# Optimization experiments

Measured on AMD Instinct MI355X. Metric: run time of the kernel, lower is better.

Reference implementation:

```python
import jax, jax.numpy as jnp
import numpy as np

V = 4
H, W, Z = 32, 64, 13
C = 256
NH = 8
WS = (4, 4, 1)
SS = (2, 2, 0)
HID = 1024


def _layernorm(x, g, b):
    mu = jnp.mean(x, axis=-1, keepdims=True)
    var = jnp.mean((x - mu) ** 2, axis=-1, keepdims=True)
    return (x - mu) * jax.lax.rsqrt(var + 1e-5) * g + b


def setup_inputs() -> dict:
    key = jax.random.key(0)
    ks = jax.random.split(key, 12)
    B = 2
    s = 0.02
    return {
        "x_z": jax.random.normal(ks[0], (B, H, W, Z, C), jnp.float32),
        "x_q": jax.random.normal(ks[1], (B, H, W, Z, C), jnp.float32),
        "x_t": jax.random.normal(ks[2], (B, H, W, Z, C), jnp.float32),
        "x_u": jax.random.normal(ks[3], (B, H, W, Z, C), jnp.float32),
        "qkv_w": jax.random.normal(ks[4], (V, C, 3 * C), jnp.float32) * s,
        "qkv_b": jnp.zeros((V, 3 * C), jnp.float32),
        "proj_w": jax.random.normal(ks[5], (V, C, C), jnp.float32) * s,
        "proj_b": jnp.zeros((V, C), jnp.float32),
        "n1_g": jnp.ones((V, C), jnp.float32),
        "n1_b": jnp.zeros((V, C), jnp.float32),
        "n2_g": jnp.ones((V, C), jnp.float32),
        "n2_b": jnp.zeros((V, C), jnp.float32),
        "fc1_w": jax.random.normal(ks[6], (V, C, HID), jnp.float32) * s,
        "fc1_b": jnp.zeros((V, HID), jnp.float32),
        "fc2_w": jax.random.normal(ks[7], (V, HID, C), jnp.float32) * s,
        "fc2_b": jnp.zeros((V, C), jnp.float32),
    }


def reference(x_z, x_q, x_t, x_u, qkv_w, qkv_b, proj_w, proj_b,
              n1_g, n1_b, n2_g, n2_b, fc1_w, fc1_b, fc2_w, fc2_b):
    x = jnp.stack([x_z, x_q, x_t, x_u], axis=0)  # [V,B,H,W,Z,C]
    B = x.shape[1]
    L = H * W * Z
    w0, w1, w2 = WS
    N = w0 * w1 * w2
    hd = C // NH
    scale = hd ** -0.5

    shortcut = x.reshape(V, B, L, C)
    xn = _layernorm(shortcut, n1_g[:, None, None, :], n1_b[:, None, None, :])
    xs = xn.reshape(V, B, H, W, Z, C)
    # cyclic shift (same sign used for both rolls in the source)
    xs = jnp.roll(xs, shift=SS, axis=(2, 3, 4))
    # window partition -> [V, B_, N, C]
    xw = xs.reshape(V, B, H // w0, w0, W // w1, w1, Z // w2, w2, C)
    xw = xw.transpose(0, 1, 2, 4, 6, 3, 5, 7, 8).reshape(V, -1, N, C)
    B_ = xw.shape[1]

    qkv = jnp.einsum('vbnc,vcd->vbnd', xw, qkv_w) + qkv_b[:, None, None, :]
    qkv = qkv.reshape(V, B_, N, 3, NH, hd).transpose(3, 1, 0, 4, 2, 5)  # [3,B_,V,NH,N,hd]
    q, k, v = qkv[0], qkv[1], qkv[2]
    # per-(variable, head) attention: heads of different variables are concatenated
    attn = jax.nn.softmax(jnp.einsum('bvhnd,bvhmd->bvhnm', q * scale, k), axis=-1)
    ctx = jnp.einsum('bvhnm,bvhmd->bvhnd', attn, v)  # [B_,V,NH,N,hd]
    # faithful to torch reshape (B_, N, V*NH, hd) -> (B_, V*N, C): rows interleave (n, v)
    big = ctx.transpose(0, 3, 1, 2, 4).reshape(B_, V * N, C)
    y = big.reshape(B_, V, N, C).transpose(1, 0, 2, 3)  # slice [:, i*N:(i+1)*N]
    y = jnp.einsum('vbnc,vcd->vbnd', y, proj_w) + proj_b[:, None, None, :]
    # window reverse
    y = y.reshape(V, B, H // w0, W // w1, Z // w2, w0, w1, w2, C)
    y = y.transpose(0, 1, 2, 5, 3, 6, 4, 7, 8).reshape(V, B, H, W, Z, C)
    y = jnp.roll(y, shift=SS, axis=(2, 3, 4))  # same-sign roll (preserves source behavior)
    y = y.reshape(V, B, L, C)

    x2 = shortcut + y
    xm = _layernorm(x2, n2_g[:, None, None, :], n2_b[:, None, None, :])
    h = jax.nn.gelu(jnp.einsum('vblc,vcd->vbld', xm, fc1_w) + fc1_b[:, None, None, :],
                    approximate=False)
    m = jnp.einsum('vbld,vdc->vblc', h, fc2_w) + fc2_b[:, None, None, :]
    out = (x2 + m).reshape(V, B, H, W, Z, C)
    return out  # stacked per-variable outputs in variable_order
```

## Files before the change

### kernel.cpp

```cpp
#include <hip/hip_runtime.h>
#include <hip/hip_bf16.h>
#include <cstdint>
#include <cstddef>

#define DI __device__ __forceinline__

typedef __bf16 bf16_t;
typedef bf16_t bf16x8 __attribute__((ext_vector_type(8)));
typedef float f32x4 __attribute__((ext_vector_type(4)));

constexpr int Vn = 4, Bn = 2, Hn = 32, Wn = 64, Zn = 13, Cn = 256, HIDn = 1024;
constexpr int Ln = Hn * Wn * Zn;
constexpr int BWn = Bn * (Hn / 4) * (Wn / 4) * Zn;
constexpr int PB = Bn * Ln;
constexpr int ROWS = Vn * PB;

DI void gload_lds16(const void* g, void* l) {
  __builtin_amdgcn_global_load_lds(
      (const __attribute__((address_space(1))) void*)g,
      (__attribute__((address_space(3))) void*)l, 16, 0, 0);
}

DI unsigned short f2bf_bits(float f) {
  __hip_bfloat16 h = __float2bfloat16(f);
  return *reinterpret_cast<unsigned short*>(&h);
}

DI float gelu_f(float x) {
  float u = x * x;
  float w = x * fmaf(0.044715f, u, 1.0f);
  float e = __expf(-1.5957691216057308f * w);
  return x * __builtin_amdgcn_rcpf(1.0f + e);
}

__global__ __launch_bounds__(256) void transpose_tile_kernel(
    const float* __restrict__ src, __hip_bfloat16* __restrict__ dst, int K, int N) {
  __shared__ float S[64][65];
  const int n0 = blockIdx.x * 64, k0 = blockIdx.y * 64, v = blockIdx.z;
  const int tc = threadIdx.x & 63, tr = threadIdx.x >> 6;
#pragma unroll
  for (int i = 0; i < 16; ++i) {
    int kk = tr + i * 4;
    S[kk][tc] = src[((size_t)v * K + k0 + kk) * N + n0 + tc];
  }
  __syncthreads();
#pragma unroll
  for (int i = 0; i < 16; ++i) {
    int nn = tr + i * 4;
    dst[((size_t)v * N + n0 + nn) * K + k0 + tc] = __float2bfloat16(S[tc][nn]);
  }
}

__global__ __launch_bounds__(256) void ln1_kernel(
    const float* __restrict__ x0, const float* __restrict__ x1,
    const float* __restrict__ x2i, const float* __restrict__ x3,
    const float* __restrict__ g_, const float* __restrict__ b_,
    __hip_bfloat16* __restrict__ xw) {
  int gw = blockIdx.x * 4 + (threadIdx.x >> 6);
  int lane = threadIdx.x & 63;
  int v = gw / PB;
  int rem = gw - v * PB;
  int bw = rem >> 4, nn = rem & 15;
  int zb = bw % 13;
  int t = bw / 13;
  int wb = t & 15, t2 = t >> 4;
  int hb = t2 & 7, b = t2 >> 3;
  int hs = (hb * 4 + (nn >> 2) + 30) & 31;
  int wsrc = (wb * 4 + (nn & 3) + 62) & 63;
  size_t l = (size_t)(hs * 64 + wsrc) * 13 + zb;
  const float* xv = (v == 0) ? x0 : (v == 1) ? x1 : (v == 2) ? x2i : x3;
  const float* xp = xv + ((size_t)b * Ln + l) * 256;
  float4 val = *(const float4*)(xp + lane * 4);
  float s = val.x + val.y + val.z + val.w;
  float sq = val.x * val.x + val.y * val.y + val.z * val.z + val.w * val.w;
#pragma unroll
  for (int o = 32; o; o >>= 1) {
    s += __shfl_xor(s, o);
    sq += __shfl_xor(sq, o);
  }
  float mean = s * (1.0f / 256.0f);
  float var = sq * (1.0f / 256.0f) - mean * mean;
  float rstd = rsqrtf(var + 1e-5f);
  const float* gg = g_ + v * 256 + lane * 4;
  const float* bb = b_ + v * 256 + lane * 4;
  ushort4 o4;
  o4.x = f2bf_bits((val.x - mean) * rstd * gg[0] + bb[0]);
  o4.y = f2bf_bits((val.y - mean) * rstd * gg[1] + bb[1]);
  o4.z = f2bf_bits((val.z - mean) * rstd * gg[2] + bb[2]);
  o4.w = f2bf_bits((val.w - mean) * rstd * gg[3] + bb[3]);
  *reinterpret_cast<ushort4*>(xw + (size_t)gw * 256 + lane * 4) = o4;
}

__global__ __launch_bounds__(256) void ln2_kernel(
    const float* __restrict__ x2, const float* __restrict__ g_,
    const float* __restrict__ b_, __hip_bfloat16* __restrict__ xm) {
  int r = blockIdx.x * 4 + (threadIdx.x >> 6);
  int lane = threadIdx.x & 63;
  int v = r / PB;
  const float* xp = x2 + (size_t)r * 256;
  float4 val = *(const float4*)(xp + lane * 4);
  float s = val.x + val.y + val.z + val.w;
  float sq = val.x * val.x + val.y * val.y + val.z * val.z + val.w * val.w;
#pragma unroll
  for (int o = 32; o; o >>= 1) {
    s += __shfl_xor(s, o);
    sq += __shfl_xor(sq, o);
  }
  float mean = s * (1.0f / 256.0f);
  float var = sq * (1.0f / 256.0f) - mean * mean;
  float rstd = rsqrtf(var + 1e-5f);
  const float* gg = g_ + v * 256 + lane * 4;
  const float* bb = b_ + v * 256 + lane * 4;
  ushort4 o4;
  o4.x = f2bf_bits((val.x - mean) * rstd * gg[0] + bb[0]);
  o4.y = f2bf_bits((val.y - mean) * rstd * gg[1] + bb[1]);
  o4.z = f2bf_bits((val.z - mean) * rstd * gg[2] + bb[2]);
  o4.w = f2bf_bits((val.w - mean) * rstd * gg[3] + bb[3]);
  *reinterpret_cast<ushort4*>(xm + (size_t)r * 256 + lane * 4) = o4;
}

__global__ __launch_bounds__(256) void attn_kernel(
    const __hip_bfloat16* __restrict__ qkvp, __hip_bfloat16* __restrict__ ctx) {
  __shared__ float P[4][16][17];
  int b_ = blockIdx.x;
  int v = blockIdx.y;
  int wid = threadIdx.x >> 6, lane = threadIdx.x & 63;
  int lm = lane & 15, hi = lane >> 4;
  const bf16_t* base = (const bf16_t*)qkvp + (size_t)(v * BWn + b_) * 16 * 768;
  const float scale = 0.17677669529663687f;
  f32x4 zero = {0.f, 0.f, 0.f, 0.f};
#pragma unroll
  for (int hh = 0; hh < 2; ++hh) {
    int h = wid + 4 * hh;
    bf16x8 qf = *(const bf16x8*)(base + (size_t)lm * 768 + h * 32 + hi * 8);
    bf16x8 kf = *(const bf16x8*)(base + (size_t)lm * 768 + 256 + h * 32 + hi * 8);
    f32x4 s = __builtin_amdgcn_mfma_f32_16x16x32_bf16(qf, kf, zero, 0, 0, 0);
    float p0[4];
#pragma unroll
    for (int q = 0; q < 4; ++q) {
      float val = s[q] * scale;
      float mx = val;
#pragma unroll
      for (int o = 8; o >= 1; o >>= 1) mx = fmaxf(mx, __shfl_xor(mx, o));
      float e = __expf(val - mx);
      float sum = e;
#pragma unroll
      for (int o = 8; o >= 1; o >>= 1) sum += __shfl_xor(sum, o);
      p0[q] = e * __builtin_amdgcn_rcpf(sum);
    }
#pragma unroll
    for (int q = 0; q < 4; ++q) P[wid][hi * 4 + q][lm] = p0[q];
    bf16x8 pa;
#pragma unroll
    for (int j = 0; j < 8; ++j) pa[j] = (bf16_t)0.f;
    if (hi < 2) {
#pragma unroll
      for (int j = 0; j < 8; ++j) pa[j] = (bf16_t)P[wid][lm][hi * 8 + j];
    }
#pragma unroll
    for (int dh = 0; dh < 2; ++dh) {
      bf16x8 vf;
#pragma unroll
      for (int j = 0; j < 8; ++j) vf[j] = (bf16_t)0.f;
      if (hi < 2) {
#pragma unroll
        for (int j = 0; j < 8; ++j)
          vf[j] = base[(size_t)(hi * 8 + j) * 768 + 512 + h * 32 + dh * 16 + lm];
      }
      f32x4 c = __builtin_amdgcn_mfma_f32_16x16x32_bf16(pa, vf, zero, 0, 0, 0);
#pragma unroll
      for (int q = 0; q < 4; ++q) {
        int n = hi * 4 + q;
        int d = dh * 16 + lm;
        int r = n * 4 + v;
        int vo = r >> 4, no = r & 15;
        ctx[((size_t)(vo * BWn + b_) * 16 + no) * 256 + h * 32 + d] = __float2bfloat16(c[q]);
      }
    }
  }
}

template <int EPI, int K, int N>
__global__ __launch_bounds__(256, 3) void gemm4(
    const __hip_bfloat16* __restrict__ A, const __hip_bfloat16* __restrict__ WT,
    const float* __restrict__ bias, __hip_bfloat16* __restrict__ outb,
    float* __restrict__ outf, const float* __restrict__ xi0,
    const float* __restrict__ xi1, const float* __restrict__ xi2,
    const float* __restrict__ xi3) {
  constexpr int NT = K / 64;
  constexpr int NC = N / 128;
  const int v = blockIdx.z;
  const int x = blockIdx.x;
  const int xcd = x & 7;
  const int j = x >> 3;
  const int c = j % NC;
  const int r = xcd + 8 * (j / NC);
  const int rowBase = r * 128;
  const int colBase = c * 128;

  const bf16_t* Av = (const bf16_t*)A + ((size_t)v * PB + rowBase) * K;
  const bf16_t* Wv = (const bf16_t*)WT + ((size_t)v * N + colBase) * K;

  __shared__ __align__(16) uint8_t smem[40960];
  bf16_t(*As)[64] = (bf16_t(*)[64])smem;
  bf16_t(*Bs)[64] = (bf16_t(*)[64])(smem + 16384);

  const int tid = threadIdx.x, wid = tid >> 6, lane = tid & 63;
  const int wr = wid >> 1, wc = wid & 1;
  const int lm = lane & 15, hi = lane >> 4;
  const int rA = lane >> 3;
  const int lg = (lane & 7) ^ rA;

  f32x4 acc[4][4];
#pragma unroll
  for (int m = 0; m < 4; ++m)
#pragma unroll
    for (int n = 0; n < 4; ++n) acc[m][n] = f32x4{0.f, 0.f, 0.f, 0.f};

  for (int t = 0; t < NT; ++t) {
    if (t) __syncthreads();
#pragma unroll
    for (int g = 0; g < 4; ++g) {
      int grp = wid * 4 + g;
      gload_lds16(Av + (size_t)(grp * 8 + rA) * K + t * 64 + lg * 8, &As[grp * 8][0]);
    }
#pragma unroll
    for (int g = 0; g < 4; ++g) {
      int grp = wid * 4 + g;
      gload_lds16(Wv + (size_t)(grp * 8 + rA) * K + t * 64 + lg * 8, &Bs[grp * 8][0]);
    }
    __syncthreads();
#pragma unroll
    for (int kk = 0; kk < 2; ++kk) {
      bf16x8 af[4], bfv[4];
#pragma unroll
      for (int m = 0; m < 4; ++m) {
        const int rr = wr * 64 + m * 16 + lm;
        af[m] = *(const bf16x8*)&As[rr][((kk * 4 + hi) ^ (lm & 7)) * 8];
      }
#pragma unroll
      for (int n = 0; n < 4; ++n) {
        const int rr = wc * 64 + n * 16 + lm;
        bfv[n] = *(const bf16x8*)&Bs[rr][((kk * 4 + hi) ^ (lm & 7)) * 8];
      }
#pragma unroll
      for (int m = 0; m < 4; ++m)
#pragma unroll
        for (int n = 0; n < 4; ++n)
          acc[m][n] = __builtin_amdgcn_mfma_f32_16x16x32_bf16(af[m], bfv[n], acc[m][n], 0, 0, 0);
    }
  }

  __syncthreads();
  uint8_t* ep = smem + wid * 10240;

  if constexpr (EPI == 0 || EPI == 2) {
    ushort(*E)[72] = (ushort(*)[72])ep;
    float bcol[4];
#pragma unroll
    for (int n = 0; n < 4; ++n) bcol[n] = bias[v * N + colBase + wc * 64 + n * 16 + lm];
#pragma unroll
    for (int m = 0; m < 4; ++m)
#pragma unroll
      for (int q = 0; q < 4; ++q) {
        int lr = m * 16 + hi * 4 + q;
#pragma unroll
        for (int n = 0; n < 4; ++n) {
          float val = acc[m][n][q] + bcol[n];
          if constexpr (EPI == 2) val = gelu_f(val);
          E[lr][n * 16 + lm] = f2bf_bits(val);
        }
      }
    const int pr = lane >> 3, pc = lane & 7;
#pragma unroll
    for (int p = 0; p < 8; ++p) {
      int lr = p * 8 + pr;
      bf16x8 val = *(const bf16x8*)&E[lr][pc * 8];
      size_t grow = (size_t)v * PB + rowBase + wr * 64 + lr;
      int gcol = colBase + wc * 64 + pc * 8;
      *(bf16x8*)&outb[grow * N + gcol] = val;
    }
  } else {
    float(*F)[36] = (float(*)[36])ep;
    const int pr = lane >> 3, pc = lane & 7;
#pragma unroll
    for (int h2 = 0; h2 < 2; ++h2) {
#pragma unroll
      for (int m = 0; m < 4; ++m)
#pragma unroll
        for (int q = 0; q < 4; ++q) {
          int lr = m * 16 + hi * 4 + q;
#pragma unroll
          for (int n2 = 0; n2 < 2; ++n2) F[lr][n2 * 16 + lm] = acc[m][h2 * 2 + n2][q];
        }
#pragma unroll
      for (int p = 0; p < 8; ++p) {
        int lr = p * 8 + pr;
        f32x4 a4 = *(const f32x4*)&F[lr][pc * 4];
        int rowv = rowBase + wr * 64 + lr;
        int gcol = colBase + wc * 64 + h2 * 32 + pc * 4;
        f32x4 b4 = *(const f32x4*)&bias[v * N + gcol];
        if constexpr (EPI == 1) {
          int b_ = rowv >> 4, nn = rowv & 15;
          int zb = b_ % 13;
          int tt = b_ / 13;
          int wb = tt & 15, tt2 = tt >> 4;
          int hb = tt2 & 7, bb = tt2 >> 3;
          int h2v = (hb * 4 + (nn >> 2) + 2) & 31;
          int w2v = (wb * 4 + (nn & 3) + 2) & 63;
          size_t l = (size_t)(h2v * 64 + w2v) * 13 + zb;
          const float* xv = (v == 0) ? xi0 : (v == 1) ? xi1 : (v == 2) ? xi2 : xi3;
          f32x4 x4 = *(const f32x4*)(xv + ((size_t)bb * Ln + l) * 256 + gcol);
          f32x4 o4 = a4 + b4 + x4;
          *(f32x4*)(outf + (((size_t)v * Bn + bb) * Ln + l) * 256 + gcol) = o4;
        } else {
          float* o = outf + ((size_t)v * PB + rowv) * 256 + gcol;
          f32x4 cur = *(const f32x4*)o;
          f32x4 o4 = cur + a4 + b4;
          *(f32x4*)o = o4;
        }
      }
      if (h2 == 0) __builtin_amdgcn_s_waitcnt(0);
    }
  }
}

extern "C" void kernel_launch(void* const* d_in, const int* in_sizes, int n_in,
                              void* d_out, int out_size, void* d_ws, size_t ws_size,
                              hipStream_t stream) {
  const float* x0 = (const float*)d_in[0];
  const float* x1 = (const float*)d_in[1];
  const float* x2i = (const float*)d_in[2];
  const float* x3 = (const float*)d_in[3];
  const float* qkv_w = (const float*)d_in[4];
  const float* qkv_b = (const float*)d_in[5];
  const float* proj_w = (const float*)d_in[6];
  const float* proj_b = (const float*)d_in[7];
  const float* n1g = (const float*)d_in[8];
  const float* n1b = (const float*)d_in[9];
  const float* n2g = (const float*)d_in[10];
  const float* n2b = (const float*)d_in[11];
  const float* fc1_w = (const float*)d_in[12];
  const float* fc1_b = (const float*)d_in[13];
  const float* fc2_w = (const float*)d_in[14];
  const float* fc2_b = (const float*)d_in[15];
  float* out = (float*)d_out;

  uint8_t* ws = (uint8_t*)d_ws;
  size_t off = 0;
  auto alloc = [&](size_t bytes) -> void* {
    void* p = ws + off;
    off += (bytes + 255) & ~(size_t)255;
    return p;
  };
  __hip_bfloat16* wqkvT = (__hip_bfloat16*)alloc((size_t)Vn * Cn * 768 * 2);
  __hip_bfloat16* wprojT = (__hip_bfloat16*)alloc((size_t)Vn * Cn * Cn * 2);
  __hip_bfloat16* wfc1T = (__hip_bfloat16*)alloc((size_t)Vn * Cn * HIDn * 2);
  __hip_bfloat16* wfc2T = (__hip_bfloat16*)alloc((size_t)Vn * HIDn * Cn * 2);
  __hip_bfloat16* xw = (__hip_bfloat16*)alloc((size_t)ROWS * Cn * 2);
  __hip_bfloat16* qkvb = (__hip_bfloat16*)alloc((size_t)ROWS * HIDn * 2);

  transpose_tile_kernel<<<dim3(768 / 64, 256 / 64, Vn), 256, 0, stream>>>(qkv_w, wqkvT, 256, 768);
  transpose_tile_kernel<<<dim3(256 / 64, 256 / 64, Vn), 256, 0, stream>>>(proj_w, wprojT, 256, 256);
  transpose_tile_kernel<<<dim3(1024 / 64, 256 / 64, Vn), 256, 0, stream>>>(fc1_w, wfc1T, 256, 1024);
  transpose_tile_kernel<<<dim3(256 / 64, 1024 / 64, Vn), 256, 0, stream>>>(fc2_w, wfc2T, 1024, 256);

  ln1_kernel<<<ROWS / 4, 256, 0, stream>>>(x0, x1, x2i, x3, n1g, n1b, xw);

  gemm4<0, 256, 768><<<dim3(416 * 6, 1, Vn), 256, 0, stream>>>(
      xw, wqkvT, qkv_b, qkvb, nullptr, nullptr, nullptr, nullptr, nullptr);

  attn_kernel<<<dim3(BWn, Vn), 256, 0, stream>>>(qkvb, xw );

  gemm4<1, 256, 256><<<dim3(416 * 2, 1, Vn), 256, 0, stream>>>(
      xw , wprojT, proj_b, nullptr, out , x0, x1, x2i, x3);

  ln2_kernel<<<ROWS / 4, 256, 0, stream>>>(out , n2g, n2b, xw );

  gemm4<2, 256, 1024><<<dim3(416 * 8, 1, Vn), 256, 0, stream>>>(
      xw , wfc1T, fc1_b, qkvb , nullptr, nullptr, nullptr, nullptr, nullptr);

  gemm4<3, 1024, 256><<<dim3(416 * 2, 1, Vn), 256, 0, stream>>>(
      qkvb , wfc2T, fc2_b, nullptr, out, nullptr, nullptr, nullptr, nullptr);
}
```

Measured before the change: 924.6 us.

## Widen GEMM tiles to 128x256 with 512-thread blocks

The GEMM kernel moves from 128x128 tiles with 4 waves to 128x256 tiles with 8 waves. Each A tile is now reused across twice as many output columns, which cuts global A traffic and halves the block count. The epilogue is split into two phases of 32 rows so it fits the per-wave LDS slice, and the explicit waitcnt between halves is dropped. Bigger blocks and launch bounds of 4 may raise register pressure and lower occupancy flexibility.

```diff
diff --git a/kernel.cpp b/kernel.cpp
--- a/kernel.cpp
+++ b/kernel.cpp
@@ -181,14 +181,14 @@
 }
 
 template <int EPI, int K, int N>
-__global__ __launch_bounds__(256, 3) void gemm4(
+__global__ __launch_bounds__(512, 4) void gemm5(
     const __hip_bfloat16* __restrict__ A, const __hip_bfloat16* __restrict__ WT,
     const float* __restrict__ bias, __hip_bfloat16* __restrict__ outb,
     float* __restrict__ outf, const float* __restrict__ xi0,
     const float* __restrict__ xi1, const float* __restrict__ xi2,
     const float* __restrict__ xi3) {
   constexpr int NT = K / 64;
-  constexpr int NC = N / 128;
+  constexpr int NC = N / 256;
   const int v = blockIdx.z;
   const int x = blockIdx.x;
   const int xcd = x & 7;
@@ -196,17 +196,17 @@
   const int c = j % NC;
   const int r = xcd + 8 * (j / NC);
   const int rowBase = r * 128;
-  const int colBase = c * 128;
+  const int colBase = c * 256;
 
   const bf16_t* Av = (const bf16_t*)A + ((size_t)v * PB + rowBase) * K;
   const bf16_t* Wv = (const bf16_t*)WT + ((size_t)v * N + colBase) * K;
 
-  __shared__ __align__(16) uint8_t smem[40960];
+  __shared__ __align__(16) uint8_t smem[49152];
   bf16_t(*As)[64] = (bf16_t(*)[64])smem;
   bf16_t(*Bs)[64] = (bf16_t(*)[64])(smem + 16384);
 
   const int tid = threadIdx.x, wid = tid >> 6, lane = tid & 63;
-  const int wr = wid >> 1, wc = wid & 1;
+  const int wr = wid >> 2, wc = wid & 3;
   const int lm = lane & 15, hi = lane >> 4;
   const int rA = lane >> 3;
   const int lg = (lane & 7) ^ rA;
@@ -220,8 +220,8 @@
   for (int t = 0; t < NT; ++t) {
     if (t) __syncthreads();
 #pragma unroll
-    for (int g = 0; g < 4; ++g) {
-      int grp = wid * 4 + g;
+    for (int g = 0; g < 2; ++g) {
+      int grp = wid * 2 + g;
       gload_lds16(Av + (size_t)(grp * 8 + rA) * K + t * 64 + lg * 8, &As[grp * 8][0]);
     }
 #pragma unroll
@@ -252,7 +252,8 @@
   }
 
   __syncthreads();
-  uint8_t* ep = smem + wid * 10240;
+  uint8_t* ep = smem + wid * 6144;
+  const int pr = lane >> 3, pc = lane & 7;
 
   if constexpr (EPI == 0 || EPI == 2) {
     ushort(*E)[72] = (ushort(*)[72])ep;
@@ -260,67 +261,74 @@
 #pragma unroll
     for (int n = 0; n < 4; ++n) bcol[n] = bias[v * N + colBase + wc * 64 + n * 16 + lm];
 #pragma unroll
-    for (int m = 0; m < 4; ++m)
-#pragma unroll
-      for (int q = 0; q < 4; ++q) {
-        int lr = m * 16 + hi * 4 + q;
-#pragma unroll
-        for (int n = 0; n < 4; ++n) {
-          float val = acc[m][n][q] + bcol[n];
-          if constexpr (EPI == 2) val = gelu_f(val);
-          E[lr][n * 16 + lm] = f2bf_bits(val);
+    for (int ph = 0; ph < 2; ++ph) {
+#pragma unroll
+      for (int mm = 0; mm < 2; ++mm) {
+        int m = ph * 2 + mm;
+#pragma unroll
+        for (int q = 0; q < 4; ++q) {
+          int lr = mm * 16 + hi * 4 + q;
+#pragma unroll
+          for (int n = 0; n < 4; ++n) {
+            float val = acc[m][n][q] + bcol[n];
+            if constexpr (EPI == 2) val = gelu_f(val);
+            E[lr][n * 16 + lm] = f2bf_bits(val);
+          }
         }
       }
-    const int pr = lane >> 3, pc = lane & 7;
-#pragma unroll
-    for (int p = 0; p < 8; ++p) {
-      int lr = p * 8 + pr;
-      bf16x8 val = *(const bf16x8*)&E[lr][pc * 8];
-      size_t grow = (size_t)v * PB + rowBase + wr * 64 + lr;
-      int gcol = colBase + wc * 64 + pc * 8;
-      *(bf16x8*)&outb[grow * N + gcol] = val;
+#pragma unroll
+      for (int p = 0; p < 4; ++p) {
+        int lr = p * 8 + pr;
+        bf16x8 valv = *(const bf16x8*)&E[lr][pc * 8];
+        size_t grow = (size_t)v * PB + rowBase + wr * 64 + ph * 32 + lr;
+        int gcol = colBase + wc * 64 + pc * 8;
+        *(bf16x8*)&outb[grow * N + gcol] = valv;
+      }
     }
   } else {
     float(*F)[36] = (float(*)[36])ep;
-    const int pr = lane >> 3, pc = lane & 7;
-#pragma unroll
-    for (int h2 = 0; h2 < 2; ++h2) {
-#pragma unroll
-      for (int m = 0; m < 4; ++m)
-#pragma unroll
-        for (int q = 0; q < 4; ++q) {
-          int lr = m * 16 + hi * 4 + q;
-#pragma unroll
-          for (int n2 = 0; n2 < 2; ++n2) F[lr][n2 * 16 + lm] = acc[m][h2 * 2 + n2][q];
+#pragma unroll
+    for (int ph = 0; ph < 2; ++ph) {
+#pragma unroll
+      for (int h2 = 0; h2 < 2; ++h2) {
+#pragma unroll
+        for (int mm = 0; mm < 2; ++mm) {
+          int m = ph * 2 + mm;
+#pragma unroll
+          for (int q = 0; q < 4; ++q) {
+            int lr = mm * 16 + hi * 4 + q;
+#pragma unroll
+            for (int n2 = 0; n2 < 2; ++n2) F[lr][n2 * 16 + lm] = acc[m][h2 * 2 + n2][q];
+          }
         }
 #pragma unroll
-      for (int p = 0; p < 8; ++p) {
-        int lr = p * 8 + pr;
-        f32x4 a4 = *(const f32x4*)&F[lr][pc * 4];
-        int rowv = rowBase + wr * 64 + lr;
-        int gcol = colBase + wc * 64 + h2 * 32 + pc * 4;
-        f32x4 b4 = *(const f32x4*)&bias[v * N + gcol];
-        if constexpr (EPI == 1) {
-          int b_ = rowv >> 4, nn = rowv & 15;
-          int zb = b_ % 13;
-          int tt = b_ / 13;
-          int wb = tt & 15, tt2 = tt >> 4;
-          int hb = tt2 & 7, bb = tt2 >> 3;
-          int h2v = (hb * 4 + (nn >> 2) + 2) & 31;
-          int w2v = (wb * 4 + (nn & 3) + 2) & 63;
-          size_t l = (size_t)(h2v * 64 + w2v) * 13 + zb;
-          const float* xv = (v == 0) ? xi0 : (v == 1) ? xi1 : (v == 2) ? xi2 : xi3;
-          f32x4 x4 = *(const f32x4*)(xv + ((size_t)bb * Ln + l) * 256 + gcol);
-          f32x4 o4 = a4 + b4 + x4;
-          *(f32x4*)(outf + (((size_t)v * Bn + bb) * Ln + l) * 256 + gcol) = o4;
-        } else {
-          float* o = outf + ((size_t)v * PB + rowv) * 256 + gcol;
-          f32x4 cur = *(const f32x4*)o;
-          f32x4 o4 = cur + a4 + b4;
-          *(f32x4*)o = o4;
+        for (int p = 0; p < 4; ++p) {
+          int lr = p * 8 + pr;
+          f32x4 a4 = *(const f32x4*)&F[lr][pc * 4];
+          int rowv = rowBase + wr * 64 + ph * 32 + lr;
+          int gcol = colBase + wc * 64 + h2 * 32 + pc * 4;
+          f32x4 b4 = *(const f32x4*)&bias[v * N + gcol];
+          if constexpr (EPI == 1) {
+            int b_ = rowv >> 4, nn = rowv & 15;
+            int zb = b_ % 13;
+            int tt = b_ / 13;
+            int wb = tt & 15, tt2 = tt >> 4;
+            int hb = tt2 & 7, bb = tt2 >> 3;
+            int h2v = (hb * 4 + (nn >> 2) + 2) & 31;
+            int w2v = (wb * 4 + (nn & 3) + 2) & 63;
+            size_t l = (size_t)(h2v * 64 + w2v) * 13 + zb;
+            const float* xv = (v == 0) ? xi0 : (v == 1) ? xi1 : (v == 2) ? xi2 : xi3;
+            f32x4 x4 = *(const f32x4*)(xv + ((size_t)bb * Ln + l) * 256 + gcol);
+            f32x4 o4 = a4 + b4 + x4;
+            *(f32x4*)(outf + (((size_t)v * Bn + bb) * Ln + l) * 256 + gcol) = o4;
+          } else {
+            float* o = outf + ((size_t)v * PB + rowv) * 256 + gcol;
+            f32x4 cur = *(const f32x4*)o;
+            f32x4 o4 = cur + a4 + b4;
+            *(f32x4*)o = o4;
+          }
         }
       }
-      if (h2 == 0) __builtin_amdgcn_s_waitcnt(0);
     }
   }
 }
@@ -367,19 +375,19 @@
 
   ln1_kernel<<<ROWS / 4, 256, 0, stream>>>(x0, x1, x2i, x3, n1g, n1b, xw);
 
-  gemm4<0, 256, 768><<<dim3(416 * 6, 1, Vn), 256, 0, stream>>>(
+  gemm5<0, 256, 768><<<dim3(416 * 3, 1, Vn), 512, 0, stream>>>(
       xw, wqkvT, qkv_b, qkvb, nullptr, nullptr, nullptr, nullptr, nullptr);
 
   attn_kernel<<<dim3(BWn, Vn), 256, 0, stream>>>(qkvb, xw );
 
-  gemm4<1, 256, 256><<<dim3(416 * 2, 1, Vn), 256, 0, stream>>>(
+  gemm5<1, 256, 256><<<dim3(416, 1, Vn), 512, 0, stream>>>(
       xw , wprojT, proj_b, nullptr, out , x0, x1, x2i, x3);
 
   ln2_kernel<<<ROWS / 4, 256, 0, stream>>>(out , n2g, n2b, xw );
 
-  gemm4<2, 256, 1024><<<dim3(416 * 8, 1, Vn), 256, 0, stream>>>(
+  gemm5<2, 256, 1024><<<dim3(416 * 4, 1, Vn), 512, 0, stream>>>(
       xw , wfc1T, fc1_b, qkvb , nullptr, nullptr, nullptr, nullptr, nullptr);
 
-  gemm4<3, 1024, 256><<<dim3(416 * 2, 1, Vn), 256, 0, stream>>>(
+  gemm5<3, 1024, 256><<<dim3(416, 1, Vn), 512, 0, stream>>>(
       qkvb , wfc2T, fc2_b, nullptr, out, nullptr, nullptr, nullptr, nullptr);
 }
```

After: 1.007 ms. +8.9%, slower.

## Fuse LayerNorm2, FC1+GELU and FC2 into one MLP kernel

Applied to the files above, without the earlier changes.

Replaces the separate ln2 kernel and two MLP GEMMs with one kernel. Each 512-thread block normalizes 128 rows into LDS, computes the hidden layer in 128-column chunks with GELU kept in LDS, and accumulates FC2 into registers. This removes the global round trip of the 1024-wide bf16 hidden activation and two launches. In exchange it uses 128KB of LDS, which limits each CU to one block, and runs with little overlap between weight loads and MFMA because every stage is separated by barriers.

```diff
diff --git a/kernel.cpp b/kernel.cpp
--- a/kernel.cpp
+++ b/kernel.cpp
@@ -91,34 +91,6 @@
   *reinterpret_cast<ushort4*>(xw + (size_t)gw * 256 + lane * 4) = o4;
 }
 
-__global__ __launch_bounds__(256) void ln2_kernel(
-    const float* __restrict__ x2, const float* __restrict__ g_,
-    const float* __restrict__ b_, __hip_bfloat16* __restrict__ xm) {
-  int r = blockIdx.x * 4 + (threadIdx.x >> 6);
-  int lane = threadIdx.x & 63;
-  int v = r / PB;
-  const float* xp = x2 + (size_t)r * 256;
-  float4 val = *(const float4*)(xp + lane * 4);
-  float s = val.x + val.y + val.z + val.w;
-  float sq = val.x * val.x + val.y * val.y + val.z * val.z + val.w * val.w;
-#pragma unroll
-  for (int o = 32; o; o >>= 1) {
-    s += __shfl_xor(s, o);
-    sq += __shfl_xor(sq, o);
-  }
-  float mean = s * (1.0f / 256.0f);
-  float var = sq * (1.0f / 256.0f) - mean * mean;
-  float rstd = rsqrtf(var + 1e-5f);
-  const float* gg = g_ + v * 256 + lane * 4;
-  const float* bb = b_ + v * 256 + lane * 4;
-  ushort4 o4;
-  o4.x = f2bf_bits((val.x - mean) * rstd * gg[0] + bb[0]);
-  o4.y = f2bf_bits((val.y - mean) * rstd * gg[1] + bb[1]);
-  o4.z = f2bf_bits((val.z - mean) * rstd * gg[2] + bb[2]);
-  o4.w = f2bf_bits((val.w - mean) * rstd * gg[3] + bb[3]);
-  *reinterpret_cast<ushort4*>(xm + (size_t)r * 256 + lane * 4) = o4;
-}
-
 __global__ __launch_bounds__(256) void attn_kernel(
     const __hip_bfloat16* __restrict__ qkvp, __hip_bfloat16* __restrict__ ctx) {
   __shared__ float P[4][16][17];
@@ -254,7 +226,7 @@
   __syncthreads();
   uint8_t* ep = smem + wid * 10240;
 
-  if constexpr (EPI == 0 || EPI == 2) {
+  if constexpr (EPI == 0) {
     ushort(*E)[72] = (ushort(*)[72])ep;
     float bcol[4];
 #pragma unroll
@@ -265,11 +237,7 @@
       for (int q = 0; q < 4; ++q) {
         int lr = m * 16 + hi * 4 + q;
 #pragma unroll
-        for (int n = 0; n < 4; ++n) {
-          float val = acc[m][n][q] + bcol[n];
-          if constexpr (EPI == 2) val = gelu_f(val);
-          E[lr][n * 16 + lm] = f2bf_bits(val);
-        }
+        for (int n = 0; n < 4; ++n) E[lr][n * 16 + lm] = f2bf_bits(acc[m][n][q] + bcol[n]);
       }
     const int pr = lane >> 3, pc = lane & 7;
 #pragma unroll
@@ -300,28 +268,219 @@
         int rowv = rowBase + wr * 64 + lr;
         int gcol = colBase + wc * 64 + h2 * 32 + pc * 4;
         f32x4 b4 = *(const f32x4*)&bias[v * N + gcol];
-        if constexpr (EPI == 1) {
-          int b_ = rowv >> 4, nn = rowv & 15;
-          int zb = b_ % 13;
-          int tt = b_ / 13;
-          int wb = tt & 15, tt2 = tt >> 4;
-          int hb = tt2 & 7, bb = tt2 >> 3;
-          int h2v = (hb * 4 + (nn >> 2) + 2) & 31;
-          int w2v = (wb * 4 + (nn & 3) + 2) & 63;
-          size_t l = (size_t)(h2v * 64 + w2v) * 13 + zb;
-          const float* xv = (v == 0) ? xi0 : (v == 1) ? xi1 : (v == 2) ? xi2 : xi3;
-          f32x4 x4 = *(const f32x4*)(xv + ((size_t)bb * Ln + l) * 256 + gcol);
-          f32x4 o4 = a4 + b4 + x4;
-          *(f32x4*)(outf + (((size_t)v * Bn + bb) * Ln + l) * 256 + gcol) = o4;
-        } else {
-          float* o = outf + ((size_t)v * PB + rowv) * 256 + gcol;
-          f32x4 cur = *(const f32x4*)o;
-          f32x4 o4 = cur + a4 + b4;
-          *(f32x4*)o = o4;
+        int b_ = rowv >> 4, nn = rowv & 15;
+        int zb = b_ % 13;
+        int tt = b_ / 13;
+        int wb = tt & 15, tt2 = tt >> 4;
+        int hb = tt2 & 7, bb = tt2 >> 3;
+        int h2v = (hb * 4 + (nn >> 2) + 2) & 31;
+        int w2v = (wb * 4 + (nn & 3) + 2) & 63;
+        size_t l = (size_t)(h2v * 64 + w2v) * 13 + zb;
+        const float* xv = (v == 0) ? xi0 : (v == 1) ? xi1 : (v == 2) ? xi2 : xi3;
+        f32x4 x4 = *(const f32x4*)(xv + ((size_t)bb * Ln + l) * 256 + gcol);
+        f32x4 o4 = a4 + b4 + x4;
+        *(f32x4*)(outf + (((size_t)v * Bn + bb) * Ln + l) * 256 + gcol) = o4;
+      }
+      if (h2 == 0) __builtin_amdgcn_s_waitcnt(0);
+    }
+  }
+}
+
+__global__ __launch_bounds__(512, 1) void mlp_fused(
+    const float* __restrict__ x2,
+    const __hip_bfloat16* __restrict__ W1T,
+    const __hip_bfloat16* __restrict__ W2T,
+    const float* __restrict__ b1, const float* __restrict__ b2,
+    const float* __restrict__ g2, const float* __restrict__ bt2,
+    float* __restrict__ outp) {
+  const int v = blockIdx.z;
+  const size_t gRow0 = (size_t)v * PB + (size_t)blockIdx.x * 128;
+
+  __shared__ __align__(16) uint8_t smem[131072];
+  uint8_t* regA = smem;
+  uint8_t* regH = smem + 65536;
+  uint8_t* regC = smem + 98304;
+
+  const int tid = threadIdx.x, wid = tid >> 6, lane = tid & 63;
+  const int lm = lane & 15, hi = lane >> 4;
+  const int wr = wid >> 1;
+  const int wc = wid & 1;
+
+  const float* gg = g2 + v * 256;
+  const float* gb = bt2 + v * 256;
+  {
+    float g4[4], b4l[4];
+#pragma unroll
+    for (int e = 0; e < 4; ++e) { g4[e] = gg[lane * 4 + e]; b4l[e] = gb[lane * 4 + e]; }
+    for (int i = 0; i < 16; ++i) {
+      int row = wid * 16 + i;
+      const float* xp = x2 + (gRow0 + row) * 256;
+      float4 val = *(const float4*)(xp + lane * 4);
+      float s = val.x + val.y + val.z + val.w;
+      float sq = val.x * val.x + val.y * val.y + val.z * val.z + val.w * val.w;
+#pragma unroll
+      for (int o = 32; o; o >>= 1) {
+        s += __shfl_xor(s, o);
+        sq += __shfl_xor(sq, o);
+      }
+      float mean = s * (1.0f / 256.0f);
+      float var = sq * (1.0f / 256.0f) - mean * mean;
+      float rstd = rsqrtf(var + 1e-5f);
+      ushort4 o4;
+      o4.x = f2bf_bits((val.x - mean) * rstd * g4[0] + b4l[0]);
+      o4.y = f2bf_bits((val.y - mean) * rstd * g4[1] + b4l[1]);
+      o4.z = f2bf_bits((val.z - mean) * rstd * g4[2] + b4l[2]);
+      o4.w = f2bf_bits((val.w - mean) * rstd * g4[3] + b4l[3]);
+      int pg = (lane >> 1) ^ (row & 7);
+      *(ushort4*)(regA + row * 512 + pg * 16 + (lane & 1) * 8) = o4;
+    }
+  }
+  __syncthreads();
+
+  bf16x8 afx[2][4][2];
+#pragma unroll
+  for (int mm = 0; mm < 2; ++mm)
+#pragma unroll
+    for (int t = 0; t < 4; ++t)
+#pragma unroll
+      for (int kk = 0; kk < 2; ++kk) {
+        int row = wr * 32 + mm * 16 + lm;
+        int g = t * 8 + kk * 4 + hi;
+        int pg = g ^ (row & 7);
+        afx[mm][t][kk] = *(const bf16x8*)(regA + row * 512 + pg * 16);
+      }
+  __syncthreads();
+
+  f32x4 acc2[2][8];
+#pragma unroll
+  for (int mm = 0; mm < 2; ++mm)
+#pragma unroll
+    for (int nn = 0; nn < 8; ++nn) acc2[mm][nn] = f32x4{0.f, 0.f, 0.f, 0.f};
+
+  const bf16_t* W1v = (const bf16_t*)W1T + (size_t)v * 1024 * 256;
+  const bf16_t* W2v = (const bf16_t*)W2T + (size_t)v * 256 * 1024;
+
+  for (int hc = 0; hc < 8; ++hc) {
+#pragma unroll
+    for (int rd = 0; rd < 8; ++rd) {
+      int s = (rd * 8 + wid) * 64 + lane;
+      int row = s >> 5, pg = s & 31;
+      int g = pg ^ (row & 7);
+      gload_lds16(W1v + (size_t)(hc * 128 + row) * 256 + g * 8, regA + (rd * 8 + wid) * 1024);
+    }
+#pragma unroll
+    for (int rd = 0; rd < 4; ++rd) {
+      int s = (rd * 8 + wid) * 64 + lane;
+      int col = s >> 3, pg = s & 7;
+      int g = pg ^ (col & 7);
+      gload_lds16(W2v + (size_t)col * 1024 + hc * 128 + g * 8, regC + (rd * 8 + wid) * 1024);
+    }
+    __syncthreads();
+
+    f32x4 acc1[2][4];
+#pragma unroll
+    for (int mm = 0; mm < 2; ++mm)
+#pragma unroll
+      for (int nn = 0; nn < 4; ++nn) acc1[mm][nn] = f32x4{0.f, 0.f, 0.f, 0.f};
+#pragma unroll
+    for (int t = 0; t < 4; ++t)
+#pragma unroll
+      for (int kk = 0; kk < 2; ++kk) {
+        bf16x8 wf[4];
+#pragma unroll
+        for (int nn = 0; nn < 4; ++nn) {
+          int row = wc * 64 + nn * 16 + lm;
+          int g = t * 8 + kk * 4 + hi;
+          int pg = g ^ (row & 7);
+          wf[nn] = *(const bf16x8*)(regA + row * 512 + pg * 16);
         }
-      }
-      if (h2 == 0) __builtin_amdgcn_s_waitcnt(0);
-    }
+#pragma unroll
+        for (int mm = 0; mm < 2; ++mm)
+#pragma unroll
+          for (int nn = 0; nn < 4; ++nn)
+            acc1[mm][nn] =
+                __builtin_amdgcn_mfma_f32_16x16x32_bf16(afx[mm][t][kk], wf[nn], acc1[mm][nn], 0, 0, 0);
+      }
+
+    float b1c[4];
+#pragma unroll
+    for (int nn = 0; nn < 4; ++nn) b1c[nn] = b1[v * 1024 + hc * 128 + wc * 64 + nn * 16 + lm];
+#pragma unroll
+    for (int mm = 0; mm < 2; ++mm)
+#pragma unroll
+      for (int nn = 0; nn < 4; ++nn)
+#pragma unroll
+        for (int q = 0; q < 4; ++q) {
+          int row = wr * 32 + mm * 16 + hi * 4 + q;
+          int col = wc * 64 + nn * 16 + lm;
+          float val = gelu_f(acc1[mm][nn][q] + b1c[nn]);
+          int pg = (col >> 3) ^ (row & 7);
+          *(ushort*)(regH + row * 256 + pg * 16 + (col & 7) * 2) = f2bf_bits(val);
+        }
+    __syncthreads();
+
+#pragma unroll
+    for (int t2 = 0; t2 < 2; ++t2) {
+      if (t2 == 1) {
+        __syncthreads();
+#pragma unroll
+        for (int rd = 0; rd < 4; ++rd) {
+          int s = (rd * 8 + wid) * 64 + lane;
+          int col = s >> 3, pg = s & 7;
+          int g = pg ^ (col & 7);
+          gload_lds16(W2v + (size_t)col * 1024 + hc * 128 + 64 + g * 8, regC + (rd * 8 + wid) * 1024);
+        }
+        __syncthreads();
+      }
+#pragma unroll
+      for (int kk = 0; kk < 2; ++kk) {
+        bf16x8 hf[2];
+#pragma unroll
+        for (int mm = 0; mm < 2; ++mm) {
+          int row = wr * 32 + mm * 16 + lm;
+          int g = t2 * 8 + kk * 4 + hi;
+          int pg = g ^ (row & 7);
+          hf[mm] = *(const bf16x8*)(regH + row * 256 + pg * 16);
+        }
+#pragma unroll
+        for (int nn = 0; nn < 8; ++nn) {
+          int col = wc * 128 + nn * 16 + lm;
+          int g = kk * 4 + hi;
+          int pg = g ^ (col & 7);
+          bf16x8 w2f = *(const bf16x8*)(regC + col * 128 + pg * 16);
+#pragma unroll
+          for (int mm = 0; mm < 2; ++mm)
+            acc2[mm][nn] = __builtin_amdgcn_mfma_f32_16x16x32_bf16(hf[mm], w2f, acc2[mm][nn], 0, 0, 0);
+        }
+      }
+    }
+    __syncthreads();
+  }
+
+  float(*F)[36] = (float(*)[36])(smem + wid * 8192);
+  const int pr = lane >> 3, pc = lane & 7;
+#pragma unroll
+  for (int ps = 0; ps < 4; ++ps) {
+#pragma unroll
+    for (int mm = 0; mm < 2; ++mm)
+#pragma unroll
+      for (int q = 0; q < 4; ++q) {
+        int lr = mm * 16 + hi * 4 + q;
+#pragma unroll
+        for (int n2 = 0; n2 < 2; ++n2) F[lr][n2 * 16 + lm] = acc2[mm][ps * 2 + n2][q];
+      }
+#pragma unroll
+    for (int p = 0; p < 4; ++p) {
+      int lr = p * 8 + pr;
+      f32x4 a4 = *(const f32x4*)&F[lr][pc * 4];
+      size_t grow = gRow0 + wr * 32 + lr;
+      int gcol = wc * 128 + ps * 32 + pc * 4;
+      f32x4 b4 = *(const f32x4*)&b2[v * 256 + gcol];
+      float* o = outp + grow * 256 + gcol;
+      f32x4 cur = *(const f32x4*)o;
+      *(f32x4*)o = cur + a4 + b4;
+    }
+    __builtin_amdgcn_s_waitcnt(0);
   }
 }
 
@@ -358,7 +517,7 @@
   __hip_bfloat16* wfc1T = (__hip_bfloat16*)alloc((size_t)Vn * Cn * HIDn * 2);
   __hip_bfloat16* wfc2T = (__hip_bfloat16*)alloc((size_t)Vn * HIDn * Cn * 2);
   __hip_bfloat16* xw = (__hip_bfloat16*)alloc((size_t)ROWS * Cn * 2);
-  __hip_bfloat16* qkvb = (__hip_bfloat16*)alloc((size_t)ROWS * HIDn * 2);
+  __hip_bfloat16* qkvb = (__hip_bfloat16*)alloc((size_t)ROWS * 768 * 2);
 
   transpose_tile_kernel<<<dim3(768 / 64, 256 / 64, Vn), 256, 0, stream>>>(qkv_w, wqkvT, 256, 768);
   transpose_tile_kernel<<<dim3(256 / 64, 256 / 64, Vn), 256, 0, stream>>>(proj_w, wprojT, 256, 256);
@@ -375,11 +534,6 @@
   gemm4<1, 256, 256><<<dim3(416 * 2, 1, Vn), 256, 0, stream>>>(
       xw , wprojT, proj_b, nullptr, out , x0, x1, x2i, x3);
 
-  ln2_kernel<<<ROWS / 4, 256, 0, stream>>>(out , n2g, n2b, xw );
-
-  gemm4<2, 256, 1024><<<dim3(416 * 8, 1, Vn), 256, 0, stream>>>(
-      xw , wfc1T, fc1_b, qkvb , nullptr, nullptr, nullptr, nullptr, nullptr);
-
-  gemm4<3, 1024, 256><<<dim3(416 * 2, 1, Vn), 256, 0, stream>>>(
-      qkvb , wfc2T, fc2_b, nullptr, out, nullptr, nullptr, nullptr, nullptr);
-}
+  mlp_fused<<<dim3(416, 1, Vn), 512, 0, stream>>>(
+      out , wfc1T, wfc2T, fc1_b, fc2_b, n2g, n2b, out);
+}
```

Result: no change. 919.0 us (-0.6%).

## Fuse LN2, FC1+GELU and FC2 into a single MLP kernel

Applied to the files above, without the earlier changes.

Replaces the separate ln2 kernel and the two MLP GEMM launches with one kernel. Each block normalizes 64 rows into LDS, then loops over 32-wide hidden chunks, computing FC1+GELU into LDS and accumulating FC2 in registers. The bf16 hidden activation no longer makes a round trip through global memory, and two launches go away. In exchange, every block re-streams the full FC1 and FC2 weights in small chunks with several barriers per chunk. The FC1 tiles are only 16x16 per wave, so MFMA utilization and latency hiding may be worse than in the tiled GEMMs.

```diff
diff --git a/kernel.cpp b/kernel.cpp
--- a/kernel.cpp
+++ b/kernel.cpp
@@ -91,34 +91,6 @@
   *reinterpret_cast<ushort4*>(xw + (size_t)gw * 256 + lane * 4) = o4;
 }
 
-__global__ __launch_bounds__(256) void ln2_kernel(
-    const float* __restrict__ x2, const float* __restrict__ g_,
-    const float* __restrict__ b_, __hip_bfloat16* __restrict__ xm) {
-  int r = blockIdx.x * 4 + (threadIdx.x >> 6);
-  int lane = threadIdx.x & 63;
-  int v = r / PB;
-  const float* xp = x2 + (size_t)r * 256;
-  float4 val = *(const float4*)(xp + lane * 4);
-  float s = val.x + val.y + val.z + val.w;
-  float sq = val.x * val.x + val.y * val.y + val.z * val.z + val.w * val.w;
-#pragma unroll
-  for (int o = 32; o; o >>= 1) {
-    s += __shfl_xor(s, o);
-    sq += __shfl_xor(sq, o);
-  }
-  float mean = s * (1.0f / 256.0f);
-  float var = sq * (1.0f / 256.0f) - mean * mean;
-  float rstd = rsqrtf(var + 1e-5f);
-  const float* gg = g_ + v * 256 + lane * 4;
-  const float* bb = b_ + v * 256 + lane * 4;
-  ushort4 o4;
-  o4.x = f2bf_bits((val.x - mean) * rstd * gg[0] + bb[0]);
-  o4.y = f2bf_bits((val.y - mean) * rstd * gg[1] + bb[1]);
-  o4.z = f2bf_bits((val.z - mean) * rstd * gg[2] + bb[2]);
-  o4.w = f2bf_bits((val.w - mean) * rstd * gg[3] + bb[3]);
-  *reinterpret_cast<ushort4*>(xm + (size_t)r * 256 + lane * 4) = o4;
-}
-
 __global__ __launch_bounds__(256) void attn_kernel(
     const __hip_bfloat16* __restrict__ qkvp, __hip_bfloat16* __restrict__ ctx) {
   __shared__ float P[4][16][17];
@@ -254,7 +226,7 @@
   __syncthreads();
   uint8_t* ep = smem + wid * 10240;
 
-  if constexpr (EPI == 0 || EPI == 2) {
+  if constexpr (EPI == 0) {
     ushort(*E)[72] = (ushort(*)[72])ep;
     float bcol[4];
 #pragma unroll
@@ -265,11 +237,7 @@
       for (int q = 0; q < 4; ++q) {
         int lr = m * 16 + hi * 4 + q;
 #pragma unroll
-        for (int n = 0; n < 4; ++n) {
-          float val = acc[m][n][q] + bcol[n];
-          if constexpr (EPI == 2) val = gelu_f(val);
-          E[lr][n * 16 + lm] = f2bf_bits(val);
-        }
+        for (int n = 0; n < 4; ++n) E[lr][n * 16 + lm] = f2bf_bits(acc[m][n][q] + bcol[n]);
       }
     const int pr = lane >> 3, pc = lane & 7;
 #pragma unroll
@@ -300,27 +268,170 @@
         int rowv = rowBase + wr * 64 + lr;
         int gcol = colBase + wc * 64 + h2 * 32 + pc * 4;
         f32x4 b4 = *(const f32x4*)&bias[v * N + gcol];
-        if constexpr (EPI == 1) {
-          int b_ = rowv >> 4, nn = rowv & 15;
-          int zb = b_ % 13;
-          int tt = b_ / 13;
-          int wb = tt & 15, tt2 = tt >> 4;
-          int hb = tt2 & 7, bb = tt2 >> 3;
-          int h2v = (hb * 4 + (nn >> 2) + 2) & 31;
-          int w2v = (wb * 4 + (nn & 3) + 2) & 63;
-          size_t l = (size_t)(h2v * 64 + w2v) * 13 + zb;
-          const float* xv = (v == 0) ? xi0 : (v == 1) ? xi1 : (v == 2) ? xi2 : xi3;
-          f32x4 x4 = *(const f32x4*)(xv + ((size_t)bb * Ln + l) * 256 + gcol);
-          f32x4 o4 = a4 + b4 + x4;
-          *(f32x4*)(outf + (((size_t)v * Bn + bb) * Ln + l) * 256 + gcol) = o4;
-        } else {
-          float* o = outf + ((size_t)v * PB + rowv) * 256 + gcol;
-          f32x4 cur = *(const f32x4*)o;
-          f32x4 o4 = cur + a4 + b4;
-          *(f32x4*)o = o4;
-        }
+        int b_ = rowv >> 4, nn = rowv & 15;
+        int zb = b_ % 13;
+        int tt = b_ / 13;
+        int wb = tt & 15, tt2 = tt >> 4;
+        int hb = tt2 & 7, bb = tt2 >> 3;
+        int h2v = (hb * 4 + (nn >> 2) + 2) & 31;
+        int w2v = (wb * 4 + (nn & 3) + 2) & 63;
+        size_t l = (size_t)(h2v * 64 + w2v) * 13 + zb;
+        const float* xv = (v == 0) ? xi0 : (v == 1) ? xi1 : (v == 2) ? xi2 : xi3;
+        f32x4 x4 = *(const f32x4*)(xv + ((size_t)bb * Ln + l) * 256 + gcol);
+        f32x4 o4 = a4 + b4 + x4;
+        *(f32x4*)(outf + (((size_t)v * Bn + bb) * Ln + l) * 256 + gcol) = o4;
       }
       if (h2 == 0) __builtin_amdgcn_s_waitcnt(0);
+    }
+  }
+}
+
+__global__ __launch_bounds__(512, 4) void mlp_fused2(
+    const float* __restrict__ x2,
+    const __hip_bfloat16* __restrict__ W1T,
+    const __hip_bfloat16* __restrict__ W2T,
+    const float* __restrict__ b1, const float* __restrict__ b2,
+    const float* __restrict__ g2, const float* __restrict__ bt2,
+    float* __restrict__ outp) {
+  const int v = blockIdx.z;
+  const size_t gRow0 = (size_t)v * PB + (size_t)blockIdx.x * 64;
+
+  __shared__ __align__(16) uint8_t smem[69632];
+  uint8_t* W1c = smem + 32768;
+  uint8_t* W2c = smem + 49152;
+  uint8_t* hbuf = smem + 65536;
+
+  const int tid = threadIdx.x, wid = tid >> 6, lane = tid & 63;
+  const int lm = lane & 15, hi = lane >> 4;
+  const int wa = wid >> 2;
+  const int wb = wid & 3;
+
+  {
+    const float* gg = g2 + v * 256;
+    const float* gb = bt2 + v * 256;
+    float g4[4], b4l[4];
+#pragma unroll
+    for (int e = 0; e < 4; ++e) { g4[e] = gg[lane * 4 + e]; b4l[e] = gb[lane * 4 + e]; }
+    for (int i = 0; i < 8; ++i) {
+      int row = wid * 8 + i;
+      const float* xp = x2 + (gRow0 + row) * 256;
+      float4 val = *(const float4*)(xp + lane * 4);
+      float s = val.x + val.y + val.z + val.w;
+      float sq = val.x * val.x + val.y * val.y + val.z * val.z + val.w * val.w;
+#pragma unroll
+      for (int o = 32; o; o >>= 1) {
+        s += __shfl_xor(s, o);
+        sq += __shfl_xor(sq, o);
+      }
+      float mean = s * (1.0f / 256.0f);
+      float var = sq * (1.0f / 256.0f) - mean * mean;
+      float rstd = rsqrtf(var + 1e-5f);
+      ushort4 o4;
+      o4.x = f2bf_bits((val.x - mean) * rstd * g4[0] + b4l[0]);
+      o4.y = f2bf_bits((val.y - mean) * rstd * g4[1] + b4l[1]);
+      o4.z = f2bf_bits((val.z - mean) * rstd * g4[2] + b4l[2]);
+      o4.w = f2bf_bits((val.w - mean) * rstd * g4[3] + b4l[3]);
+      int t = hi;
+      int g = (lane >> 1) & 7;
+      int p = row * 4 + t;
+      int gp = g ^ ((row & 1) * 4 + t);
+      *(ushort4*)(smem + p * 128 + gp * 16 + (lane & 1) * 8) = o4;
+    }
+  }
+  __syncthreads();
+
+  bf16x8 xnf[4][2];
+#pragma unroll
+  for (int t = 0; t < 4; ++t)
+#pragma unroll
+    for (int kk = 0; kk < 2; ++kk) {
+      int row = wb * 16 + lm;
+      int p = row * 4 + t;
+      int gp = (kk * 4 + hi) ^ ((row & 1) * 4 + t);
+      xnf[t][kk] = *(const bf16x8*)(smem + p * 128 + gp * 16);
+    }
+
+  f32x4 acc2[8];
+#pragma unroll
+  for (int ca = 0; ca < 8; ++ca) acc2[ca] = f32x4{0.f, 0.f, 0.f, 0.f};
+
+  const bf16_t* W1v = (const bf16_t*)W1T + (size_t)v * 1024 * 256;
+  const bf16_t* W2v = (const bf16_t*)W2T + (size_t)v * 256 * 1024;
+  const int l8 = lane >> 3;
+  const int lg = (lane & 7) ^ l8;
+
+  for (int hc = 0; hc < 32; ++hc) {
+    if (hc) __syncthreads();
+#pragma unroll
+    for (int s = 0; s < 2; ++s) {
+      int i = wid * 2 + s;
+      int p = i * 8 + l8;
+      gload_lds16(W1v + (size_t)(hc * 32 + (p >> 2)) * 256 + (p & 3) * 64 + lg * 8,
+                  W1c + i * 1024);
+    }
+#pragma unroll
+    for (int s = 0; s < 2; ++s) {
+      int i = wid * 2 + s;
+      int p = i * 8 + l8;
+      gload_lds16(W2v + (size_t)(p * 2 + (lg >> 2)) * 1024 + hc * 32 + (lg & 3) * 8,
+                  W2c + i * 1024);
+    }
+    __syncthreads();
+
+    f32x4 acc1 = f32x4{0.f, 0.f, 0.f, 0.f};
+#pragma unroll
+    for (int t = 0; t < 4; ++t)
+#pragma unroll
+      for (int kk = 0; kk < 2; ++kk) {
+        int hrow = wa * 16 + lm;
+        int p = hrow * 4 + t;
+        int gp = (kk * 4 + hi) ^ ((hrow & 1) * 4 + t);
+        bf16x8 w1f = *(const bf16x8*)(W1c + p * 128 + gp * 16);
+        acc1 = __builtin_amdgcn_mfma_f32_16x16x32_bf16(w1f, xnf[t][kk], acc1, 0, 0, 0);
+      }
+
+    {
+      f32x4 b1v = *(const f32x4*)&b1[v * 1024 + hc * 32 + wa * 16 + hi * 4];
+      ushort4 hp;
+      hp.x = f2bf_bits(gelu_f(acc1[0] + b1v[0]));
+      hp.y = f2bf_bits(gelu_f(acc1[1] + b1v[1]));
+      hp.z = f2bf_bits(gelu_f(acc1[2] + b1v[2]));
+      hp.w = f2bf_bits(gelu_f(acc1[3] + b1v[3]));
+      int row = wb * 16 + lm;
+      int p = row >> 1;
+      int gl = (row & 1) * 4 + wa * 2 + (hi >> 1);
+      int gp = gl ^ (p & 7);
+      *(ushort4*)(hbuf + p * 128 + gp * 16 + (hi & 1) * 8) = hp;
+    }
+    __syncthreads();
+
+    {
+      int row = wb * 16 + lm;
+      int p = row >> 1;
+      int gp = ((row & 1) * 4 + hi) ^ (p & 7);
+      bf16x8 hf = *(const bf16x8*)(hbuf + p * 128 + gp * 16);
+#pragma unroll
+      for (int ca = 0; ca < 8; ++ca) {
+        int col = wa * 128 + ca * 16 + lm;
+        int p2 = col >> 1;
+        int gp2 = ((col & 1) * 4 + hi) ^ (p2 & 7);
+        bf16x8 w2f = *(const bf16x8*)(W2c + p2 * 128 + gp2 * 16);
+        acc2[ca] = __builtin_amdgcn_mfma_f32_16x16x32_bf16(w2f, hf, acc2[ca], 0, 0, 0);
+      }
+    }
+  }
+
+  {
+    size_t orow = gRow0 + wb * 16 + lm;
+    float* obase = outp + orow * 256;
+#pragma unroll
+    for (int ca = 0; ca < 8; ++ca) {
+      int col = wa * 128 + ca * 16 + hi * 4;
+      f32x4 b4 = *(const f32x4*)&b2[v * 256 + col];
+      float* o = obase + col;
+      f32x4 cur = *(const f32x4*)o;
+      f32x4 res = cur + acc2[ca] + b4;
+      *(f32x4*)o = res;
     }
   }
 }
@@ -358,7 +469,7 @@
   __hip_bfloat16* wfc1T = (__hip_bfloat16*)alloc((size_t)Vn * Cn * HIDn * 2);
   __hip_bfloat16* wfc2T = (__hip_bfloat16*)alloc((size_t)Vn * HIDn * Cn * 2);
   __hip_bfloat16* xw = (__hip_bfloat16*)alloc((size_t)ROWS * Cn * 2);
-  __hip_bfloat16* qkvb = (__hip_bfloat16*)alloc((size_t)ROWS * HIDn * 2);
+  __hip_bfloat16* qkvb = (__hip_bfloat16*)alloc((size_t)ROWS * 768 * 2);
 
   transpose_tile_kernel<<<dim3(768 / 64, 256 / 64, Vn), 256, 0, stream>>>(qkv_w, wqkvT, 256, 768);
   transpose_tile_kernel<<<dim3(256 / 64, 256 / 64, Vn), 256, 0, stream>>>(proj_w, wprojT, 256, 256);
@@ -375,11 +486,6 @@
   gemm4<1, 256, 256><<<dim3(416 * 2, 1, Vn), 256, 0, stream>>>(
       xw , wprojT, proj_b, nullptr, out , x0, x1, x2i, x3);
 
-  ln2_kernel<<<ROWS / 4, 256, 0, stream>>>(out , n2g, n2b, xw );
-
-  gemm4<2, 256, 1024><<<dim3(416 * 8, 1, Vn), 256, 0, stream>>>(
-      xw , wfc1T, fc1_b, qkvb , nullptr, nullptr, nullptr, nullptr, nullptr);
-
-  gemm4<3, 1024, 256><<<dim3(416 * 2, 1, Vn), 256, 0, stream>>>(
-      qkvb , wfc2T, fc2_b, nullptr, out, nullptr, nullptr, nullptr, nullptr);
-}
+  mlp_fused2<<<dim3(PB / 64, 1, Vn), 512, 0, stream>>>(
+      out , wfc1T, wfc2T, fc1_b, fc2_b, n2g, n2b, out);
+}
```

After: 938.7 us. About the same (+1.5%).
